# Optimization experiments

Hardware: AMD Instinct MI355X
Metric: run time of the kernel (lower is better)

Reference implementation:

```python
import jax, jax.numpy as jnp
from jax import lax
import numpy as np

S, B, T = 64, 128, 32
V_SRC, V_TRG, E, HE, HD = 32000, 32000, 256, 512, 512
PAD, SOS, EOS = 0, 1, 2


def setup_inputs() -> dict:
    key = jax.random.key(0)
    ks = jax.random.split(key, 32)
    p = lambda k, sh, s=0.05: (jax.random.normal(k, sh, jnp.float32) * s)
    inp = {
        # tokens avoid PAD/SOS/EOS so src_len == S everywhere (no packing needed)
        "src": jax.random.randint(ks[0], (S, B), 3, V_SRC).astype(jnp.int32),
        "src_len": jnp.full((B,), S, dtype=jnp.int32),
        "trg": jax.random.randint(ks[1], (T, B), 3, V_TRG).astype(jnp.int32),
        # embeddings
        "emb_enc": p(ks[2], (V_SRC, E)),
        "emb_dec": p(ks[3], (V_TRG, E)),
        # encoder bidirectional GRU (torch layout: W_ih [3H, in], W_hh [3H, H])
        "Wih_f": p(ks[4], (3 * HE, E)), "Whh_f": p(ks[5], (3 * HE, HE)),
        "bih_f": p(ks[6], (3 * HE,)),  "bhh_f": p(ks[7], (3 * HE,)),
        "Wih_b": p(ks[8], (3 * HE, E)), "Whh_b": p(ks[9], (3 * HE, HE)),
        "bih_b": p(ks[10], (3 * HE,)), "bhh_b": p(ks[11], (3 * HE,)),
        # enc->dec hidden bridge: Linear(2*HE, HD)
        "W_fc": p(ks[12], (HD, 2 * HE)), "b_fc": p(ks[13], (HD,)),
        # attention: Linear(HD + 2*HE, HD) on cat(hid, enc_out), then v [HD]
        "W_attn": p(ks[14], (HD, HD + 2 * HE)), "b_attn": p(ks[15], (HD,)),
        "v_attn": p(ks[16], (HD,)),
        # decoder GRU: input cat(emb, weighted) -> E + 2*HE
        "Wih_d": p(ks[17], (3 * HD, E + 2 * HE)), "Whh_d": p(ks[18], (3 * HD, HD)),
        "bih_d": p(ks[19], (3 * HD,)), "bhh_d": p(ks[20], (3 * HD,)),
        # fc_out: Linear(HD + 2*HE + E, V)
        "W_out": p(ks[21], (V_TRG, HD + 2 * HE + E)), "b_out": p(ks[22], (V_TRG,)),
    }
    return inp


def _gru_step(W_ih, W_hh, b_ih, b_hh):
    def step(h, x):
        gi = x @ W_ih.T + b_ih
        gh = h @ W_hh.T + b_hh
        ir, iz, i_n = jnp.split(gi, 3, axis=-1)
        hr, hz, h_n = jnp.split(gh, 3, axis=-1)
        r = jax.nn.sigmoid(ir + hr)
        z = jax.nn.sigmoid(iz + hz)
        n = jnp.tanh(i_n + r * h_n)
        h2 = (1.0 - z) * n + z * h
        return h2, h2
    return step


def reference(src, src_len, trg, emb_enc, emb_dec,
              Wih_f, Whh_f, bih_f, bhh_f, Wih_b, Whh_b, bih_b, bhh_b,
              W_fc, b_fc, W_attn, b_attn, v_attn,
              Wih_d, Whh_d, bih_d, bhh_d, W_out, b_out):
    b = src.shape[1]
    he = Whh_f.shape[1]
    hd = Whh_d.shape[1]
    vocab = W_out.shape[0]
    t_len = trg.shape[0]

    # ---- encoder: bidirectional GRU ----
    emb = emb_enc[src]                               # [S, B, E]
    h0 = jnp.zeros((b, he), emb.dtype)
    hf, outs_f = lax.scan(_gru_step(Wih_f, Whh_f, bih_f, bhh_f), h0, emb)
    hb, outs_b = lax.scan(_gru_step(Wih_b, Whh_b, bih_b, bhh_b), h0, emb[::-1])
    enc_outs = jnp.concatenate([outs_f, outs_b[::-1]], axis=-1)   # [S, B, 2HE]
    hid = jnp.tanh(jnp.concatenate([hf, hb], -1) @ W_fc.T + b_fc)  # [B, HD]

    # ---- attention precompute ----
    mask = (src != PAD).T                             # [B, S]
    enc_b = enc_outs.transpose(1, 0, 2)               # [B, S, 2HE]
    W_a_h, W_a_e = W_attn[:, :hd], W_attn[:, hd:]     # split cat(hid, enc_out)
    enc_proj = jnp.einsum('bse,de->bsd', enc_b, W_a_e) + b_attn  # [B, S, HD]

    gru_d = _gru_step(Wih_d, Whh_d, bih_d, bhh_d)

    def dec_step(h, tok):
        e = emb_dec[tok]                              # [B, E]
        energy = jnp.tanh(enc_proj + (h @ W_a_h.T)[:, None, :])
        scores = jnp.einsum('bsd,d->bs', energy, v_attn)
        scores = jnp.where(mask, scores, -1e10)
        a = jax.nn.softmax(scores, axis=1)
        w = jnp.einsum('bs,bse->be', a, enc_b)        # [B, 2HE]
        h2, _ = gru_d(h, jnp.concatenate([e, w], -1))
        logits = jnp.concatenate([h2, w, e], -1) @ W_out.T + b_out
        return h2, jax.nn.log_softmax(logits, axis=1)

    # teacher forcing (tf_ratio = 1.0): decoder inputs are trg[0..T-2]
    _, logps = lax.scan(dec_step, hid, trg[:-1])      # [T-1, B, V]

    outs = jnp.zeros((t_len, b, vocab), logps.dtype).at[:, :, EOS].set(100.0)
    outs = outs.at[:t_len - 1].set(logps)
    return outs
```

## Files before the change

kernel.cpp:

```cpp
#include <hip/hip_runtime.h>
#include <cstddef>
#include <cstdint>

#define S_LEN 64
#define BATCH 128
#define T_LEN 32
#define E_DIM 256
#define VOCAB 32000
#define XDIM 1792
#define MPAD 4096

typedef unsigned short bfu;
typedef short short8 __attribute__((ext_vector_type(8)));
typedef float f32x4 __attribute__((ext_vector_type(4)));

__device__ __forceinline__ bfu f2b(float f) {
    unsigned int x = __float_as_uint(f);
    x += 0x7fffu + ((x >> 16) & 1u);
    return (bfu)(x >> 16);
}
__device__ __forceinline__ float b2f(bfu u) { return __uint_as_float(((unsigned)u) << 16); }
__device__ __forceinline__ f32x4 MFMA16(short8 a, short8 b, f32x4 c) {
    return __builtin_amdgcn_mfma_f32_16x16x32_bf16(a, b, c, 0, 0, 0);
}
__device__ __forceinline__ float sigm(float x) {
    return 1.f / (1.f + exp2f(x * -1.4426950408889634f));
}
__device__ __forceinline__ float ftanh(float x) {
    float xc = fminf(15.f, fmaxf(-15.f, x));
    float t = exp2f(xc * 2.8853900817779268f);
    return (t - 1.f) / (t + 1.f);
}

#define GLDS(gsrc, ldst)                                                       \
    __builtin_amdgcn_global_load_lds(                                          \
        (const __attribute__((address_space(1))) void*)(gsrc),                 \
        (__attribute__((address_space(3))) void*)(ldst), 16, 0, 0)

__global__ void zero_kernel(float* __restrict__ p, int n) {
    int i = blockIdx.x * 256 + threadIdx.x;
    if (i < n) p[i] = 0.f;
}

__global__ void conv_all(
    const float* __restrict__ s0, const float* __restrict__ s1,
    const float* __restrict__ s2, const float* __restrict__ s3,
    const float* __restrict__ s4, const float* __restrict__ s5,
    const float* __restrict__ s6, const float* __restrict__ s7,
    const float* __restrict__ s8,
    bfu* __restrict__ d0, bfu* __restrict__ d1, bfu* __restrict__ d2,
    bfu* __restrict__ d3, bfu* __restrict__ d4, bfu* __restrict__ d5,
    bfu* __restrict__ d6, bfu* __restrict__ d7, bfu* __restrict__ d8)
{
    int i = blockIdx.x * 256 + threadIdx.x;
    if (i >= 15941632) return;
    const float* s; bfu* d; int base;
    if      (i <   98304) { s = s0; d = d0; base = 0; }
    else if (i <  196608) { s = s1; d = d1; base = 98304; }
    else if (i <  393216) { s = s2; d = d2; base = 196608; }
    else if (i <  589824) { s = s3; d = d3; base = 393216; }
    else if (i <  720896) { s = s4; d = d4; base = 589824; }
    else if (i <  917504) { s = s5; d = d5; base = 720896; }
    else if (i < 1409024) { s = s6; d = d6; base = 917504; }
    else if (i < 1605632) { s = s7; d = d7; base = 1409024; }
    else                  { s = s8; d = d8; base = 1605632; }
    int j = i - base;
    float4 v = ((const float4*)s)[j];
    ushort4 o;
    o.x = f2b(v.x); o.y = f2b(v.y); o.z = f2b(v.z); o.w = f2b(v.w);
    ((ushort4*)d)[j] = o;
}

__global__ void gather_emb(const float* __restrict__ table, const int* __restrict__ idx,
                           bfu* __restrict__ out, int total) {
    int i = blockIdx.x * 256 + threadIdx.x;
    if (i >= total) return;
    int row = i >> 8, k = i & 255;
    out[i] = f2b(table[(size_t)idx[row] * E_DIM + k]);
}

__global__ void gather_trg(const float* __restrict__ table, const int* __restrict__ trg,
                           bfu* __restrict__ Xb, int total) {
    int i = blockIdx.x * 256 + threadIdx.x;
    if (i >= total) return;
    int row = i >> 8, k = i & 255;
    Xb[(size_t)row * XDIM + 1536 + k] = f2b(table[(size_t)trg[row] * E_DIM + k]);
}

__global__ __launch_bounds__(256) void gemm_bf16(
    const bfu* __restrict__ A0, int lda0, const bfu* __restrict__ W0, int ldw0,
    float* __restrict__ C0, int ldc0, const float* __restrict__ bias0, int K0,
    const bfu* __restrict__ A1, int lda1, const bfu* __restrict__ W1, int ldw1,
    float* __restrict__ C1, int ldc1, const float* __restrict__ bias1, int K1,
    int act, bfu* __restrict__ Cb0)
{
    const int z = blockIdx.z;
    const bfu* A = z ? A1 : A0;
    const bfu* W = z ? W1 : W0;
    float*     C = z ? C1 : C0;
    const float* bias = z ? bias1 : bias0;
    bfu*       Cb = z ? nullptr : Cb0;
    const int lda = z ? lda1 : lda0;
    const int ldw = z ? ldw1 : ldw0;
    const int ldc = z ? ldc1 : ldc0;
    const int K   = z ? K1 : K0;

    __shared__ short lds[2][2][4096];
    const int tid  = threadIdx.x;
    const int wid  = tid >> 6, lane = tid & 63;
    const int l15  = lane & 15, lk = lane >> 4;
    const int wr   = (wid >> 1) * 64, wc = (wid & 1) * 64;
    const size_t row0 = (size_t)blockIdx.y * 128;
    const size_t col0 = (size_t)blockIdx.x * 128;

    const int r0 = tid & 127, kc0 = tid >> 7;
    const int kc1 = kc0 + 2;
    const int sb0 = (wid * 64) * 16;
    const int sb1 = (wid * 64 + 256) * 16;

    f32x4 acc[4][4];
#pragma unroll
    for (int m = 0; m < 4; ++m)
#pragma unroll
        for (int n = 0; n < 4; ++n) acc[m][n] = (f32x4){0.f, 0.f, 0.f, 0.f};

    auto stage = [&](int buf, int kt) {
        char* ba = (char*)&lds[buf][0][0];
        char* bb = (char*)&lds[buf][1][0];
        GLDS(A + (row0 + r0) * (size_t)lda + kt + kc0 * 8, ba + sb0);
        GLDS(A + (row0 + r0) * (size_t)lda + kt + kc1 * 8, ba + sb1);
        GLDS(W + (col0 + r0) * (size_t)ldw + kt + kc0 * 8, bb + sb0);
        GLDS(W + (col0 + r0) * (size_t)ldw + kt + kc1 * 8, bb + sb1);
    };

    stage(0, 0);
    __syncthreads();
    const int nk = K >> 5;
    for (int t = 0; t < nk; ++t) {
        const int buf = t & 1;
        if (t + 1 < nk) stage(buf ^ 1, (t + 1) << 5);
        short8 af[4], bf_[4];
#pragma unroll
        for (int m = 0; m < 4; ++m)
            af[m] = *(const short8*)&lds[buf][0][lk * 1024 + (wr + m * 16 + l15) * 8];
#pragma unroll
        for (int n = 0; n < 4; ++n)
            bf_[n] = *(const short8*)&lds[buf][1][lk * 1024 + (wc + n * 16 + l15) * 8];
#pragma unroll
        for (int m = 0; m < 4; ++m)
#pragma unroll
            for (int n = 0; n < 4; ++n)
                acc[m][n] = MFMA16(af[m], bf_[n], acc[m][n]);
        __syncthreads();
    }

    float bv[4];
#pragma unroll
    for (int n = 0; n < 4; ++n)
        bv[n] = bias ? bias[col0 + wc + n * 16 + l15] : 0.f;
    const size_t crow = row0 + wr + lk * 4;
#pragma unroll
    for (int m = 0; m < 4; ++m) {
#pragma unroll
        for (int q = 0; q < 4; ++q) {
            const size_t r = crow + m * 16 + q;
            float* cp = C + r * ldc + col0 + wc + l15;
            bfu*   cb = Cb ? (Cb + r * ldc + col0 + wc + l15) : nullptr;
#pragma unroll
            for (int n = 0; n < 4; ++n) {
                float v = acc[m][n][q] + bv[n];
                if (act) v = ftanh(v);
                cp[n * 16] = v;
                if (Cb) cb[n * 16] = f2b(v);
            }
        }
    }
}

__global__ __launch_bounds__(512) void gemm_big(
    const bfu* __restrict__ A, const bfu* __restrict__ W,
    float* __restrict__ C, const float* __restrict__ bias,
    bfu* __restrict__ Lb, int obf)
{
    __shared__ short lds[2][2][8192];
    const int tid = threadIdx.x;
    const int wid = tid >> 6, lane = tid & 63;
    const int l15 = lane & 15, lk = lane >> 4;
    const int wr = (wid >> 2) * 128;
    const int wcc = (wid & 3) * 64;
    const int fid = blockIdx.x;
    const int bx = fid >> 4, by = fid & 15;
    const size_t row0 = (size_t)by * 256;
    const size_t col0 = (size_t)bx * 256;

    f32x4 acc[8][4];
#pragma unroll
    for (int m = 0; m < 8; ++m)
#pragma unroll
        for (int n = 0; n < 4; ++n) acc[m][n] = (f32x4){0.f, 0.f, 0.f, 0.f};

    auto stage = [&](int buf, int kt) {
        char* ba = (char*)&lds[buf][0][0];
        char* bb = (char*)&lds[buf][1][0];
#pragma unroll
        for (int it = 0; it < 2; ++it) {
            int c = it * 512 + tid;
            int kc = c >> 8, row = c & 255;
            int base = (it * 512 + wid * 64) * 16;
            GLDS(A + (row0 + row) * (size_t)XDIM + kt + kc * 8, ba + base);
            GLDS(W + (col0 + row) * (size_t)XDIM + kt + kc * 8, bb + base);
        }
    };

    stage(0, 0);
    __syncthreads();
    for (int t = 0; t < 56; ++t) {
        const int buf = t & 1;
        if (t < 55) stage(buf ^ 1, (t + 1) * 32);
        short8 af[8], bf_[4];
#pragma unroll
        for (int m = 0; m < 8; ++m)
            af[m] = *(const short8*)&lds[buf][0][lk * 2048 + (wr + m * 16 + l15) * 8];
#pragma unroll
        for (int n = 0; n < 4; ++n)
            bf_[n] = *(const short8*)&lds[buf][1][lk * 2048 + (wcc + n * 16 + l15) * 8];
#pragma unroll
        for (int m = 0; m < 8; ++m)
#pragma unroll
            for (int n = 0; n < 4; ++n)
                acc[m][n] = MFMA16(af[m], bf_[n], acc[m][n]);
        __syncthreads();
    }
    if (row0 + wr < 3968) {
        float bv[4];
#pragma unroll
        for (int n = 0; n < 4; ++n) bv[n] = bias[col0 + wcc + n * 16 + l15];
#pragma unroll
        for (int m = 0; m < 8; ++m) {
#pragma unroll
            for (int q = 0; q < 4; ++q) {
                const size_t r = row0 + wr + lk * 4 + m * 16 + q;
                if (obf) {
                    bfu* cp = Lb + r * VOCAB + col0 + wcc + l15;
#pragma unroll
                    for (int n = 0; n < 4; ++n) {
                        unsigned hb = f2b(acc[m][n][q] + bv[n]);
                        unsigned ot = (unsigned)__shfl_xor((int)hb, 1);
                        if ((lane & 1) == 0)
                            *(unsigned*)(cp + n * 16) = (hb & 0xffffu) | (ot << 16);
                    }
                } else {
                    float* cp = C + r * VOCAB + col0 + wcc + l15;
#pragma unroll
                    for (int n = 0; n < 4; ++n) cp[n * 16] = acc[m][n][q] + bv[n];
                }
            }
        }
    }
}

__global__ __launch_bounds__(256) void enc_step(
    const float* __restrict__ gi_f, const float* __restrict__ gi_b,
    const bfu* __restrict__ Whhf_b, const bfu* __restrict__ Whhb_b,
    const float* __restrict__ bhh_f, const float* __restrict__ bhh_b,
    const float* __restrict__ hin, float* __restrict__ hout,
    const bfu* __restrict__ hbin, bfu* __restrict__ hbout,
    bfu* __restrict__ encbt, int s)
{
    __shared__ short Bs[64 * 48 * 8];
    const int tid = threadIdx.x;
    const int wid = tid >> 6, lane = tid & 63;
    const int l15 = lane & 15, lk = lane >> 4;
    const int dir = blockIdx.z;
    const int u0 = blockIdx.x * 16;
    const int p = dir ? (S_LEN - 1 - s) : s;
    const bfu* Whh = dir ? Whhb_b : Whhf_b;
    const float* bhh = dir ? bhh_b : bhh_f;
    const float* gi = (dir ? gi_b : gi_f) + (size_t)p * BATCH * 1536;

    {
        char* bb = (char*)Bs;
#pragma unroll
        for (int it = 0; it < 12; ++it) {
            int c = it * 256 + tid;
            int r48 = c % 48, kc = c / 48;
            int wr = (r48 >> 4) * 512 + u0 + (r48 & 15);
            GLDS(Whh + (size_t)wr * 512 + kc * 8, bb + (it * 256 + wid * 64) * 16);
        }
    }
    __syncthreads();

    const bfu* ap0 = hbin + (size_t)(wid * 32 + l15) * 1024 + dir * 512 + lk * 8;
    const bfu* ap1 = ap0 + (size_t)16 * 1024;
    f32x4 acc[2][3];
#pragma unroll
    for (int m = 0; m < 2; ++m)
#pragma unroll
        for (int g = 0; g < 3; ++g) acc[m][g] = (f32x4){0.f, 0.f, 0.f, 0.f};

#pragma unroll
    for (int kk = 0; kk < 16; ++kk) {
        short8 a0 = *(const short8*)(ap0 + kk * 32);
        short8 a1 = *(const short8*)(ap1 + kk * 32);
#pragma unroll
        for (int g = 0; g < 3; ++g) {
            short8 bf_ = *(const short8*)&Bs[((kk * 4 + lk) * 48 + g * 16 + l15) * 8];
            acc[0][g] = MFMA16(a0, bf_, acc[0][g]);
            acc[1][g] = MFMA16(a1, bf_, acc[1][g]);
        }
    }

    const int u = u0 + l15;
    const float bR = bhh[u], bZ = bhh[512 + u], bN = bhh[1024 + u];
#pragma unroll
    for (int m = 0; m < 2; ++m) {
#pragma unroll
        for (int q = 0; q < 4; ++q) {
            const int b = wid * 32 + m * 16 + lk * 4 + q;
            const float* gib = gi + (size_t)b * 1536;
            float rr = sigm(gib[u] + acc[m][0][q] + bR);
            float zz = sigm(gib[512 + u] + acc[m][1][q] + bZ);
            float nn = ftanh(gib[1024 + u] + rr * (acc[m][2][q] + bN));
            float h2 = (1.f - zz) * nn + zz * hin[(size_t)b * 1024 + dir * 512 + u];
            hout[(size_t)b * 1024 + dir * 512 + u] = h2;
            hbout[(size_t)b * 1024 + dir * 512 + u] = f2b(h2);
            encbt[((size_t)b * S_LEN + p) * 1024 + dir * 512 + u] = f2b(h2);
        }
    }
}

__global__ __launch_bounds__(256) void attn_fused(
    const bfu* __restrict__ hb, const bfu* __restrict__ Wahb,
    const float* __restrict__ encp, const bfu* __restrict__ encbt,
    const float* __restrict__ v_attn, const int* __restrict__ src,
    bfu* __restrict__ wbuf, bfu* __restrict__ Xb, int t)
{
    __shared__ float hls[512];
    __shared__ float vas[512];
    __shared__ float hps[512];
    __shared__ float sc[64];
    const int b = blockIdx.x, tid = threadIdx.x;
    for (int i = tid; i < 512; i += 256) {
        hls[i] = b2f(hb[(size_t)b * 512 + i]);
        vas[i] = v_attn[i];
    }
    __syncthreads();
    for (int j = tid; j < 512; j += 256) {
        const uint4* wrow = (const uint4*)(Wahb + (size_t)j * 1536);
        float acc = 0.f;
#pragma unroll 8
        for (int k8 = 0; k8 < 64; ++k8) {
            uint4 wv = wrow[k8];
            const float* xp = &hls[k8 * 8];
            acc += __uint_as_float(wv.x << 16) * xp[0] + __uint_as_float(wv.x & 0xffff0000u) * xp[1]
                 + __uint_as_float(wv.y << 16) * xp[2] + __uint_as_float(wv.y & 0xffff0000u) * xp[3]
                 + __uint_as_float(wv.z << 16) * xp[4] + __uint_as_float(wv.z & 0xffff0000u) * xp[5]
                 + __uint_as_float(wv.w << 16) * xp[6] + __uint_as_float(wv.w & 0xffff0000u) * xp[7];
        }
        hps[j] = acc;
    }
    __syncthreads();
    const int s = tid >> 2, l4 = tid & 3;
    const float* ep = encp + ((size_t)b * S_LEN + s) * 512;
    float part = 0.f;
#pragma unroll 4
    for (int d = l4; d < 512; d += 4) part += vas[d] * ftanh(ep[d] + hps[d]);
    part += __shfl_xor(part, 1);
    part += __shfl_xor(part, 2);
    if (l4 == 0) sc[s] = (src[s * BATCH + b] != 0) ? part : -1e10f;
    __syncthreads();
    if (tid < 64) {
        float x = sc[tid], mx = x;
        for (int o = 1; o < 64; o <<= 1) mx = fmaxf(mx, __shfl_xor(mx, o));
        float e = expf(x - mx), s2 = e;
        for (int o = 1; o < 64; o <<= 1) s2 += __shfl_xor(s2, o);
        sc[tid] = e / s2;
    }
    __syncthreads();
    bfu* xw = Xb + ((size_t)t * BATCH + b) * XDIM + 512;
#pragma unroll
    for (int c = 0; c < 4; ++c) {
        int e = tid + 256 * c;
        float a2 = 0.f;
#pragma unroll 8
        for (int s2 = 0; s2 < S_LEN; ++s2) a2 += sc[s2] * b2f(encbt[((size_t)b * S_LEN + s2) * 1024 + e]);
        bfu v = f2b(a2);
        wbuf[(size_t)b * 1024 + e] = v;
        xw[e] = v;
    }
}

__global__ __launch_bounds__(256) void dec_step(
    const float* __restrict__ gie, const bfu* __restrict__ Whhd_b,
    const bfu* __restrict__ Wihd_b, const float* __restrict__ bhh_d,
    const bfu* __restrict__ hbin, const bfu* __restrict__ wbuf,
    const float* __restrict__ hin, float* __restrict__ hout,
    bfu* __restrict__ hbout, bfu* __restrict__ Xb, int t)
{
    __shared__ short Bh[64 * 48 * 8];
    __shared__ short Bw[128 * 48 * 8];
    const int tid = threadIdx.x;
    const int wid = tid >> 6, lane = tid & 63;
    const int l15 = lane & 15, lk = lane >> 4;
    const int u0 = blockIdx.x * 16;

    {
        char* bb = (char*)Bh;
#pragma unroll
        for (int it = 0; it < 12; ++it) {
            int c = it * 256 + tid;
            int r48 = c % 48, kc = c / 48;
            int wr = (r48 >> 4) * 512 + u0 + (r48 & 15);
            GLDS(Whhd_b + (size_t)wr * 512 + kc * 8, bb + (it * 256 + wid * 64) * 16);
        }
        char* bw = (char*)Bw;
#pragma unroll
        for (int it = 0; it < 24; ++it) {
            int c = it * 256 + tid;
            int r48 = c % 48, kc = c / 48;
            int wr = (r48 >> 4) * 512 + u0 + (r48 & 15);
            GLDS(Wihd_b + (size_t)wr * 1280 + 256 + kc * 8, bw + (it * 256 + wid * 64) * 16);
        }
    }
    __syncthreads();

    f32x4 accR[2], accZ[2], accNH[2], accNW[2];
#pragma unroll
    for (int m = 0; m < 2; ++m) {
        accR[m] = (f32x4){0.f, 0.f, 0.f, 0.f};
        accZ[m] = (f32x4){0.f, 0.f, 0.f, 0.f};
        accNH[m] = (f32x4){0.f, 0.f, 0.f, 0.f};
        accNW[m] = (f32x4){0.f, 0.f, 0.f, 0.f};
    }

    {
        const bfu* ap0 = hbin + (size_t)(wid * 32 + l15) * 512 + lk * 8;
        const bfu* ap1 = ap0 + (size_t)16 * 512;
#pragma unroll
        for (int kk = 0; kk < 16; ++kk) {
            short8 a0 = *(const short8*)(ap0 + kk * 32);
            short8 a1 = *(const short8*)(ap1 + kk * 32);
            short8 br = *(const short8*)&Bh[((kk * 4 + lk) * 48 + l15) * 8];
            short8 bz = *(const short8*)&Bh[((kk * 4 + lk) * 48 + 16 + l15) * 8];
            short8 bn = *(const short8*)&Bh[((kk * 4 + lk) * 48 + 32 + l15) * 8];
            accR[0] = MFMA16(a0, br, accR[0]);
            accR[1] = MFMA16(a1, br, accR[1]);
            accZ[0] = MFMA16(a0, bz, accZ[0]);
            accZ[1] = MFMA16(a1, bz, accZ[1]);
            accNH[0] = MFMA16(a0, bn, accNH[0]);
            accNH[1] = MFMA16(a1, bn, accNH[1]);
        }
    }
    {
        const bfu* ap0 = wbuf + (size_t)(wid * 32 + l15) * 1024 + lk * 8;
        const bfu* ap1 = ap0 + (size_t)16 * 1024;
#pragma unroll
        for (int kk = 0; kk < 32; ++kk) {
            short8 a0 = *(const short8*)(ap0 + kk * 32);
            short8 a1 = *(const short8*)(ap1 + kk * 32);
            short8 br = *(const short8*)&Bw[((kk * 4 + lk) * 48 + l15) * 8];
            short8 bz = *(const short8*)&Bw[((kk * 4 + lk) * 48 + 16 + l15) * 8];
            short8 bn = *(const short8*)&Bw[((kk * 4 + lk) * 48 + 32 + l15) * 8];
            accR[0] = MFMA16(a0, br, accR[0]);
            accR[1] = MFMA16(a1, br, accR[1]);
            accZ[0] = MFMA16(a0, bz, accZ[0]);
            accZ[1] = MFMA16(a1, bz, accZ[1]);
            accNW[0] = MFMA16(a0, bn, accNW[0]);
            accNW[1] = MFMA16(a1, bn, accNW[1]);
        }
    }

    const int u = u0 + l15;
    const float bR = bhh_d[u], bZ = bhh_d[512 + u], bN = bhh_d[1024 + u];
#pragma unroll
    for (int m = 0; m < 2; ++m) {
#pragma unroll
        for (int q = 0; q < 4; ++q) {
            const int b = wid * 32 + m * 16 + lk * 4 + q;
            const float* geb = gie + ((size_t)t * BATCH + b) * 1536;
            float rr = sigm(geb[u] + accR[m][q] + bR);
            float zz = sigm(geb[512 + u] + accZ[m][q] + bZ);
            float nn = ftanh(geb[1024 + u] + accNW[m][q] + rr * (accNH[m][q] + bN));
            float h2 = (1.f - zz) * nn + zz * hin[(size_t)b * 512 + u];
            hout[(size_t)b * 512 + u] = h2;
            hbout[(size_t)b * 512 + u] = f2b(h2);
            Xb[((size_t)t * BATCH + b) * XDIM + u] = f2b(h2);
        }
    }
}

__global__ __launch_bounds__(256) void log_softmax_fill(
    const bfu* __restrict__ Lb, float* __restrict__ out, int obf)
{
    __shared__ float sm[256], ss[256];
    const int row = blockIdx.x;
    const int tid = threadIdx.x;
    float* po = out + (size_t)row * VOCAB;
    if (row >= 3968) {
        float4* p4 = (float4*)po;
        for (int i = tid; i < 8000; i += 256) {
            float4 v = {0.f, 0.f, 0.f, 0.f};
            if (i == 0) v.z = 100.f;
            p4[i] = v;
        }
        return;
    }
    float m = -3.4e38f, ssum = 0.f;
    if (obf) {
        const uint4* pb = (const uint4*)(Lb + (size_t)row * VOCAB);
        for (int i = tid; i < 4000; i += 256) {
            uint4 w = pb[i];
            float x[8];
            x[0] = __uint_as_float(w.x << 16); x[1] = __uint_as_float(w.x & 0xffff0000u);
            x[2] = __uint_as_float(w.y << 16); x[3] = __uint_as_float(w.y & 0xffff0000u);
            x[4] = __uint_as_float(w.z << 16); x[5] = __uint_as_float(w.z & 0xffff0000u);
            x[6] = __uint_as_float(w.w << 16); x[7] = __uint_as_float(w.w & 0xffff0000u);
            float mx = x[0];
#pragma unroll
            for (int j = 1; j < 8; ++j) mx = fmaxf(mx, x[j]);
            float mn = fmaxf(m, mx);
            float e = 0.f;
#pragma unroll
            for (int j = 0; j < 8; ++j) e += expf(x[j] - mn);
            ssum = ssum * expf(m - mn) + e;
            m = mn;
        }
    } else {
        const float4* p4 = (const float4*)po;
        for (int i = tid; i < 8000; i += 256) {
            float4 v = p4[i];
            float mx = fmaxf(fmaxf(v.x, v.y), fmaxf(v.z, v.w));
            float mn = fmaxf(m, mx);
            ssum = ssum * expf(m - mn) + expf(v.x - mn) + expf(v.y - mn)
                 + expf(v.z - mn) + expf(v.w - mn);
            m = mn;
        }
    }
    sm[tid] = m; ss[tid] = ssum;
    __syncthreads();
    for (int off = 128; off > 0; off >>= 1) {
        if (tid < off) {
            float m2 = sm[tid + off], s2 = ss[tid + off];
            float M = fmaxf(sm[tid], m2);
            ss[tid] = ss[tid] * expf(sm[tid] - M) + s2 * expf(m2 - M);
            sm[tid] = M;
        }
        __syncthreads();
    }
    const float lse = sm[0] + logf(ss[0]);
    if (obf) {
        const uint4* pb = (const uint4*)(Lb + (size_t)row * VOCAB);
        float4* p4 = (float4*)po;
        for (int i = tid; i < 4000; i += 256) {
            uint4 w = pb[i];
            float4 a, b4;
            a.x = __uint_as_float(w.x << 16) - lse;
            a.y = __uint_as_float(w.x & 0xffff0000u) - lse;
            a.z = __uint_as_float(w.y << 16) - lse;
            a.w = __uint_as_float(w.y & 0xffff0000u) - lse;
            b4.x = __uint_as_float(w.z << 16) - lse;
            b4.y = __uint_as_float(w.z & 0xffff0000u) - lse;
            b4.z = __uint_as_float(w.w << 16) - lse;
            b4.w = __uint_as_float(w.w & 0xffff0000u) - lse;
            p4[i * 2] = a;
            p4[i * 2 + 1] = b4;
        }
    } else {
        float4* p4 = (float4*)po;
        for (int i = tid; i < 8000; i += 256) {
            float4 v = p4[i];
            v.x -= lse; v.y -= lse; v.z -= lse; v.w -= lse;
            p4[i] = v;
        }
    }
}

extern "C" void kernel_launch(void* const* d_in, const int* in_sizes, int n_in,
                              void* d_out, int out_size, void* d_ws, size_t ws_size,
                              hipStream_t stream)
{
    const int*   src     = (const int*)d_in[0];
    const int*   trg     = (const int*)d_in[2];
    const float* emb_enc = (const float*)d_in[3];
    const float* emb_dec = (const float*)d_in[4];
    const float* Wih_f   = (const float*)d_in[5];
    const float* Whh_f   = (const float*)d_in[6];
    const float* bih_f   = (const float*)d_in[7];
    const float* bhh_f   = (const float*)d_in[8];
    const float* Wih_b   = (const float*)d_in[9];
    const float* Whh_b   = (const float*)d_in[10];
    const float* bih_b   = (const float*)d_in[11];
    const float* bhh_b   = (const float*)d_in[12];
    const float* W_fc    = (const float*)d_in[13];
    const float* b_fc    = (const float*)d_in[14];
    const float* W_attn  = (const float*)d_in[15];
    const float* b_attn  = (const float*)d_in[16];
    const float* v_attn  = (const float*)d_in[17];
    const float* Wih_d   = (const float*)d_in[18];
    const float* Whh_d   = (const float*)d_in[19];
    const float* bih_d   = (const float*)d_in[20];
    const float* bhh_d   = (const float*)d_in[21];
    const float* W_out   = (const float*)d_in[22];
    const float* b_out   = (const float*)d_in[23];
    float* out = (float*)d_out;

    char* wsb = (char*)d_ws;
    size_t off = 0;
    auto alloc = [&](size_t bytes) { void* q = wsb + off; off = (off + bytes + 255) & ~(size_t)255; return q; };
    bfu*   emb_b   = (bfu*)alloc((size_t)8192 * 256 * 2);
    bfu*   encbt_b = (bfu*)alloc((size_t)8192 * 1024 * 2);
    float* encp    = (float*)alloc((size_t)8192 * 512 * 4);
    float* gi_f    = (float*)alloc((size_t)8192 * 1536 * 4);
    float* gi_b    = (float*)alloc((size_t)8192 * 1536 * 4);
    float* gie     = (float*)alloc((size_t)3968 * 1536 * 4);
    bfu*   wbuf    = (bfu*)alloc((size_t)128 * 1024 * 2);
    float* hA      = (float*)alloc((size_t)128 * 1024 * 4);
    float* hB      = (float*)alloc((size_t)128 * 1024 * 4);
    bfu*   hbA     = (bfu*)alloc((size_t)128 * 1024 * 2);
    bfu*   hbB     = (bfu*)alloc((size_t)128 * 1024 * 2);
    float* hdA     = (float*)alloc((size_t)128 * 512 * 4);
    float* hdB     = (float*)alloc((size_t)128 * 512 * 4);
    bfu*   hdbA    = (bfu*)alloc((size_t)128 * 512 * 2);
    bfu*   hdbB    = (bfu*)alloc((size_t)128 * 512 * 2);
    bfu*   Xb      = (bfu*)alloc((size_t)MPAD * XDIM * 2);
    bfu*   Wihf_b  = (bfu*)alloc((size_t)1536 * 256 * 2);
    bfu*   Wihb_b  = (bfu*)alloc((size_t)1536 * 256 * 2);
    bfu*   Whhf_b  = (bfu*)alloc((size_t)1536 * 512 * 2);
    bfu*   Whhb_b  = (bfu*)alloc((size_t)1536 * 512 * 2);
    bfu*   Wfc_b   = (bfu*)alloc((size_t)512 * 1024 * 2);
    bfu*   Wattn_b = (bfu*)alloc((size_t)512 * 1536 * 2);
    bfu*   Wihd_b  = (bfu*)alloc((size_t)1536 * 1280 * 2);
    bfu*   Whhd_b  = (bfu*)alloc((size_t)1536 * 512 * 2);
    bfu*   Wout_b  = (bfu*)alloc((size_t)VOCAB * XDIM * 2);

    const size_t lb_bytes = (size_t)MPAD * VOCAB * 2;
    bfu* Lb = nullptr;
    if (ws_size >= off + lb_bytes + 256) Lb = (bfu*)alloc(lb_bytes);
    const int obf = (Lb != nullptr) ? 1 : 0;

    conv_all<<<(15941632 + 255) / 256, 256, 0, stream>>>(
        Wih_f, Wih_b, Whh_f, Whh_b, W_fc, W_attn, Wih_d, Whh_d, W_out,
        Wihf_b, Wihb_b, Whhf_b, Whhb_b, Wfc_b, Wattn_b, Wihd_b, Whhd_b, Wout_b);

    gather_emb<<<(8192 * 256 + 255) / 256, 256, 0, stream>>>(emb_enc, src, emb_b, 8192 * 256);
    gather_trg<<<(3968 * 256 + 255) / 256, 256, 0, stream>>>(emb_dec, trg, Xb, 3968 * 256);
    zero_kernel<<<(131072 + 255) / 256, 256, 0, stream>>>(hA, 131072);
    zero_kernel<<<(65536 + 255) / 256, 256, 0, stream>>>((float*)hbA, 65536);

    gemm_bf16<<<dim3(12, 64, 2), 256, 0, stream>>>(
        emb_b, 256, Wihf_b, 256, gi_f, 1536, bih_f, 256,
        emb_b, 256, Wihb_b, 256, gi_b, 1536, bih_b, 256, 0, nullptr);
    gemm_bf16<<<dim3(12, 31, 1), 256, 0, stream>>>(
        Xb + 1536, XDIM, Wihd_b, 1280, gie, 1536, bih_d, 256,
        Xb + 1536, XDIM, Wihd_b, 1280, gie, 1536, bih_d, 256, 0, nullptr);

    for (int s = 0; s < S_LEN; ++s) {
        const float* hin  = (s & 1) ? hB : hA;
        float*       hout = (s & 1) ? hA : hB;
        const bfu*   hbin = (s & 1) ? hbB : hbA;
        bfu*         hbout = (s & 1) ? hbA : hbB;
        enc_step<<<dim3(32, 1, 2), 256, 0, stream>>>(
            gi_f, gi_b, Whhf_b, Whhb_b, bhh_f, bhh_b,
            hin, hout, hbin, hbout, encbt_b, s);
    }
    gemm_bf16<<<dim3(4, 1, 1), 256, 0, stream>>>(
        hbA, 1024, Wfc_b, 1024, hdA, 512, b_fc, 1024,
        hbA, 1024, Wfc_b, 1024, hdA, 512, b_fc, 1024, 1, hdbA);
    gemm_bf16<<<dim3(4, 64, 1), 256, 0, stream>>>(
        encbt_b, 1024, Wattn_b + 512, 1536, encp, 512, b_attn, 1024,
        encbt_b, 1024, Wattn_b + 512, 1536, encp, 512, b_attn, 1024, 0, nullptr);

    for (int t = 0; t < T_LEN - 1; ++t) {
        const float* hin  = (t & 1) ? hdB : hdA;
        float*       hout = (t & 1) ? hdA : hdB;
        const bfu*   hbin = (t & 1) ? hdbB : hdbA;
        bfu*         hbout = (t & 1) ? hdbA : hdbB;
        attn_fused<<<BATCH, 256, 0, stream>>>(hbin, Wattn_b, encp, encbt_b,
                                              v_attn, src, wbuf, Xb, t);
        dec_step<<<32, 256, 0, stream>>>(
            gie, Whhd_b, Wihd_b, bhh_d, hbin, wbuf, hin, hout, hbout, Xb, t);
    }

    gemm_big<<<dim3(2000, 1), 512, 0, stream>>>(Xb, Wout_b, out, b_out, Lb, obf);
    log_softmax_fill<<<4096, 256, 0, stream>>>(Lb, out, obf);
}
```

Before: 4.149 ms.

## Transpose attention hidden weights for coalesced matvec and split output GEMM launches

Measured after the change: 4.306 ms. +3.8%, slower.

```diff
diff --git a/kernel.cpp b/kernel.cpp
--- a/kernel.cpp
+++ b/kernel.cpp
@@ -71,6 +71,13 @@
     ((ushort4*)d)[j] = o;
 }
 
+__global__ void transpose_wah(const float* __restrict__ W_attn, bfu* __restrict__ WahT) {
+    int i = blockIdx.x * 256 + threadIdx.x;
+    if (i >= 262144) return;
+    int k = i >> 9, j = i & 511;
+    WahT[i] = f2b(W_attn[(size_t)j * 1536 + k]);
+}
+
 __global__ void gather_emb(const float* __restrict__ table, const int* __restrict__ idx,
                            bfu* __restrict__ out, int total) {
     int i = blockIdx.x * 256 + threadIdx.x;
@@ -180,7 +187,7 @@
 __global__ __launch_bounds__(512) void gemm_big(
     const bfu* __restrict__ A, const bfu* __restrict__ W,
     float* __restrict__ C, const float* __restrict__ bias,
-    bfu* __restrict__ Lb, int obf)
+    bfu* __restrict__ Lb, int obf, int bx0)
 {
     __shared__ short lds[2][2][8192];
     const int tid = threadIdx.x;
@@ -189,7 +196,7 @@
     const int wr = (wid >> 2) * 128;
     const int wcc = (wid & 3) * 64;
     const int fid = blockIdx.x;
-    const int bx = fid >> 4, by = fid & 15;
+    const int bx = bx0 + (fid >> 4), by = fid & 15;
     const size_t row0 = (size_t)by * 256;
     const size_t col0 = (size_t)bx * 256;
 
@@ -330,7 +337,7 @@
 }
 
 __global__ __launch_bounds__(256) void attn_fused(
-    const bfu* __restrict__ hb, const bfu* __restrict__ Wahb,
+    const bfu* __restrict__ hb, const bfu* __restrict__ WahT,
     const float* __restrict__ encp, const bfu* __restrict__ encbt,
     const float* __restrict__ v_attn, const int* __restrict__ src,
     bfu* __restrict__ wbuf, bfu* __restrict__ Xb, int t)
@@ -345,19 +352,18 @@
         vas[i] = v_attn[i];
     }
     __syncthreads();
-    for (int j = tid; j < 512; j += 256) {
-        const uint4* wrow = (const uint4*)(Wahb + (size_t)j * 1536);
-        float acc = 0.f;
+    {
+        const unsigned* wt = (const unsigned*)WahT;
+        float a0 = 0.f, a1 = 0.f;
 #pragma unroll 8
-        for (int k8 = 0; k8 < 64; ++k8) {
-            uint4 wv = wrow[k8];
-            const float* xp = &hls[k8 * 8];
-            acc += __uint_as_float(wv.x << 16) * xp[0] + __uint_as_float(wv.x & 0xffff0000u) * xp[1]
-                 + __uint_as_float(wv.y << 16) * xp[2] + __uint_as_float(wv.y & 0xffff0000u) * xp[3]
-                 + __uint_as_float(wv.z << 16) * xp[4] + __uint_as_float(wv.z & 0xffff0000u) * xp[5]
-                 + __uint_as_float(wv.w << 16) * xp[6] + __uint_as_float(wv.w & 0xffff0000u) * xp[7];
-        }
-        hps[j] = acc;
+        for (int k = 0; k < 512; ++k) {
+            unsigned w = wt[k * 256 + tid];
+            float hk = hls[k];
+            a0 += hk * __uint_as_float(w << 16);
+            a1 += hk * __uint_as_float(w & 0xffff0000u);
+        }
+        hps[tid * 2]     = a0;
+        hps[tid * 2 + 1] = a1;
     }
     __syncthreads();
     const int s = tid >> 2, l4 = tid & 3;
@@ -629,6 +635,7 @@
     bfu*   Whhb_b  = (bfu*)alloc((size_t)1536 * 512 * 2);
     bfu*   Wfc_b   = (bfu*)alloc((size_t)512 * 1024 * 2);
     bfu*   Wattn_b = (bfu*)alloc((size_t)512 * 1536 * 2);
+    bfu*   WahT    = (bfu*)alloc((size_t)512 * 512 * 2);
     bfu*   Wihd_b  = (bfu*)alloc((size_t)1536 * 1280 * 2);
     bfu*   Whhd_b  = (bfu*)alloc((size_t)1536 * 512 * 2);
     bfu*   Wout_b  = (bfu*)alloc((size_t)VOCAB * XDIM * 2);
@@ -641,6 +648,7 @@
     conv_all<<<(15941632 + 255) / 256, 256, 0, stream>>>(
         Wih_f, Wih_b, Whh_f, Whh_b, W_fc, W_attn, Wih_d, Whh_d, W_out,
         Wihf_b, Wihb_b, Whhf_b, Whhb_b, Wfc_b, Wattn_b, Wihd_b, Whhd_b, Wout_b);
+    transpose_wah<<<1024, 256, 0, stream>>>(W_attn, WahT);
 
     gather_emb<<<(8192 * 256 + 255) / 256, 256, 0, stream>>>(emb_enc, src, emb_b, 8192 * 256);
     gather_trg<<<(3968 * 256 + 255) / 256, 256, 0, stream>>>(emb_dec, trg, Xb, 3968 * 256);
@@ -675,12 +683,17 @@
         float*       hout = (t & 1) ? hdA : hdB;
         const bfu*   hbin = (t & 1) ? hdbB : hdbA;
         bfu*         hbout = (t & 1) ? hdbA : hdbB;
-        attn_fused<<<BATCH, 256, 0, stream>>>(hbin, Wattn_b, encp, encbt_b,
+        attn_fused<<<BATCH, 256, 0, stream>>>(hbin, WahT, encp, encbt_b,
                                               v_attn, src, wbuf, Xb, t);
         dec_step<<<32, 256, 0, stream>>>(
             gie, Whhd_b, Wihd_b, bhh_d, hbin, wbuf, hin, hout, hbout, Xb, t);
     }
 
-    gemm_big<<<dim3(2000, 1), 512, 0, stream>>>(Xb, Wout_b, out, b_out, Lb, obf);
+    int bx0 = 0;
+    for (int g = 0; g < 4; ++g) {
+        int nbx = (g < 3) ? 32 : 29;
+        gemm_big<<<dim3(nbx * 16, 1), 512, 0, stream>>>(Xb, Wout_b, out, b_out, Lb, obf, bx0);
+        bx0 += nbx;
+    }
     log_softmax_fill<<<4096, 256, 0, stream>>>(Lb, out, obf);
 }
```
